# Optimization experiments

Measured on AMD Instinct MI355X. Metric: run time of the kernel, lower is better.

The kernel has to match this reference:

```python
import jax, jax.numpy as jnp
import numpy as np
import math

D_MODEL = 512
N_HEADS = 8
D_K = D_MODEL // N_HEADS
D_FF = 2048
EPS = 1e-6


def _layer_norm(x, gamma, beta):
    # Matches the torch module: unbiased std (ddof=1), divide by (std + eps)
    mean = jnp.mean(x, axis=-1, keepdims=True)
    std = jnp.std(x, axis=-1, ddof=1, keepdims=True)
    return gamma * (x - mean) / (std + EPS) + beta


def setup_inputs() -> dict:
    key = jax.random.key(0)
    ks = jax.random.split(key, 16)
    B, S = 4, 2048
    s_attn = 1.0 / math.sqrt(D_MODEL)
    s_ff1 = 1.0 / math.sqrt(D_MODEL)
    s_ff2 = 1.0 / math.sqrt(D_FF)
    inp = {
        "x": jax.random.normal(ks[0], (B, S, D_MODEL), dtype=jnp.float32),
        "mask": jnp.ones((1, 1, S, S), dtype=jnp.int32),
        "wq": jax.random.normal(ks[1], (D_MODEL, D_MODEL), jnp.float32) * s_attn,
        "bq": jnp.zeros((D_MODEL,), jnp.float32),
        "wk": jax.random.normal(ks[2], (D_MODEL, D_MODEL), jnp.float32) * s_attn,
        "bk": jnp.zeros((D_MODEL,), jnp.float32),
        "wv": jax.random.normal(ks[3], (D_MODEL, D_MODEL), jnp.float32) * s_attn,
        "bv": jnp.zeros((D_MODEL,), jnp.float32),
        "wo": jax.random.normal(ks[4], (D_MODEL, D_MODEL), jnp.float32) * s_attn,
        "bo": jnp.zeros((D_MODEL,), jnp.float32),
        "w1": jax.random.normal(ks[5], (D_MODEL, D_FF), jnp.float32) * s_ff1,
        "b1": jnp.zeros((D_FF,), jnp.float32),
        "w2": jax.random.normal(ks[6], (D_FF, D_MODEL), jnp.float32) * s_ff2,
        "b2": jnp.zeros((D_MODEL,), jnp.float32),
        "g1": jnp.ones((1, 1, D_MODEL), jnp.float32),
        "be1": jnp.zeros((1, 1, D_MODEL), jnp.float32),
        "g2": jnp.ones((1, 1, D_MODEL), jnp.float32),
        "be2": jnp.zeros((1, 1, D_MODEL), jnp.float32),
    }
    return inp


def reference(x, mask, wq, bq, wk, bk, wv, bv, wo, bo, w1, b1, w2, b2, g1, be1, g2, be2):
    B, S, _ = x.shape
    # --- residual 1: pre-norm self-attention ---
    xn = _layer_norm(x, g1, be1)
    q = (xn @ wq + bq).reshape(B, S, N_HEADS, D_K).transpose(0, 2, 1, 3)
    k = (xn @ wk + bk).reshape(B, S, N_HEADS, D_K).transpose(0, 2, 1, 3)
    v = (xn @ wv + bv).reshape(B, S, N_HEADS, D_K).transpose(0, 2, 1, 3)
    # NOTE: source uses floor division `//` by sqrt(d_k) (a faithful-ly kept bug)
    scores = jnp.floor_divide(jnp.einsum("bhqd,bhkd->bhqk", q, k), math.sqrt(D_K))
    scores = jnp.where(mask == 0, jnp.float32(-1e9), scores)
    attn = jax.nn.softmax(scores, axis=-1)
    ctx = jnp.einsum("bhqk,bhkd->bhqd", attn, v)
    ctx = ctx.transpose(0, 2, 1, 3).reshape(B, S, D_MODEL)
    x = x + (ctx @ wo + bo)
    # --- residual 2: pre-norm feed-forward ---
    xn2 = _layer_norm(x, g2, be2)
    ff = jax.nn.relu(xn2 @ w1 + b1) @ w2 + b2
    return x + ff
```

## Files before the change

### kernel.cpp

```cpp
#include <hip/hip_runtime.h>
#include <cmath>

#define SEQ 2048
#define DM 512
#define DFF 2048
#define NH 8
#define DKH 64
#define NROWS 8192

typedef __attribute__((ext_vector_type(8))) short bf16x8;
typedef __attribute__((ext_vector_type(16))) float f32x16;

__device__ __forceinline__ ushort f2bf(float f) {
    uint u = __float_as_uint(f);
    u += 0x7fff + ((u >> 16) & 1);
    return (ushort)(u >> 16);
}
__device__ __forceinline__ float bf2f(ushort h) {
    return __uint_as_float(((uint)h) << 16);
}
__device__ __forceinline__ uint cvtpk_bf16(float a, float b) {
    uint r;
    asm("v_cvt_pk_bf16_f32 %0, %1, %2" : "=v"(r) : "v"(a), "v"(b));
    return r;
}
__device__ __forceinline__ void gl_lds16(const void* g, void* l) {
    __builtin_amdgcn_global_load_lds(
        (const __attribute__((address_space(1))) void*)g,
        (__attribute__((address_space(3))) void*)l, 16, 0, 0);
}
__device__ __forceinline__ void* swz(char* base, int row, int col) {
    int byte = (row << 7) + (col << 1);
    byte ^= (row & 7) << 4;
    return base + byte;
}
__device__ __forceinline__ void* swzg(char* base, int row, int k) {
    int byte = (row << 7) + (k << 1);
    byte ^= ((row >> 2) & 7) << 4;
    return base + byte;
}

template<bool SPLIT>
__global__ __launch_bounds__(64) void ln_kernel(const float* __restrict__ x,
        const float* __restrict__ g, const float* __restrict__ b,
        ushort* __restrict__ oh, ushort* __restrict__ ol) {
    int row = blockIdx.x;
    int t = threadIdx.x;
    const float* xr = x + (size_t)row * DM + t * 8;
    float v[8];
    *(float4*)&v[0] = *(const float4*)(xr);
    *(float4*)&v[4] = *(const float4*)(xr + 4);
    float s = 0.f;
    #pragma unroll
    for (int j = 0; j < 8; ++j) s += v[j];
    #pragma unroll
    for (int m = 32; m > 0; m >>= 1) s += __shfl_xor(s, m);
    float mean = s * (1.0f / DM);
    float ss = 0.f;
    #pragma unroll
    for (int j = 0; j < 8; ++j) { float d = v[j] - mean; ss += d * d; }
    #pragma unroll
    for (int m = 32; m > 0; m >>= 1) ss += __shfl_xor(ss, m);
    float inv = 1.0f / (sqrtf(ss * (1.0f / (DM - 1))) + 1e-6f);
    float gv[8], bv[8];
    *(float4*)&gv[0] = *(const float4*)(g + t * 8);
    *(float4*)&gv[4] = *(const float4*)(g + t * 8 + 4);
    *(float4*)&bv[0] = *(const float4*)(b + t * 8);
    *(float4*)&bv[4] = *(const float4*)(b + t * 8 + 4);
    union { ushort us[8]; float4 f4; } ph, pl;
    #pragma unroll
    for (int j = 0; j < 8; ++j) {
        float o = gv[j] * (v[j] - mean) * inv + bv[j];
        ushort hb = f2bf(o);
        ph.us[j] = hb;
        if (SPLIT) pl.us[j] = f2bf(o - bf2f(hb));
    }
    *(float4*)(oh + (size_t)row * DM + t * 8) = ph.f4;
    if (SPLIT) *(float4*)(ol + (size_t)row * DM + t * 8) = pl.f4;
}

template<bool SPLIT>
__global__ __launch_bounds__(256) void wconv(const float* __restrict__ W,
        ushort* __restrict__ Th, ushort* __restrict__ Tl, int K, int N) {
    __shared__ float tile[64][65];
    int k0 = blockIdx.x * 64, n0 = blockIdx.y * 64;
    int t = threadIdx.x;
    {
        int kr = t >> 2, c0 = (t & 3) * 16;
        const float* src = W + (size_t)(k0 + kr) * N + n0 + c0;
        #pragma unroll
        for (int j = 0; j < 4; ++j)
            *(float4*)&tile[kr][c0 + j * 4] = *(const float4*)(src + j * 4);
    }
    __syncthreads();
    int n = t >> 2, kc = (t & 3) * 16;
    union { ushort us[16]; float4 f4[2]; } ph, pl;
    #pragma unroll
    for (int j = 0; j < 16; ++j) {
        float v = tile[kc + j][n];
        ushort hb = f2bf(v);
        ph.us[j] = hb;
        if (SPLIT) pl.us[j] = f2bf(v - bf2f(hb));
    }
    ushort* dh = Th + (size_t)(n0 + n) * K + k0 + kc;
    *(float4*)(dh) = ph.f4[0];
    *(float4*)(dh + 8) = ph.f4[1];
    if (SPLIT) {
        ushort* dl = Tl + (size_t)(n0 + n) * K + k0 + kc;
        *(float4*)(dl) = pl.f4[0];
        *(float4*)(dl + 8) = pl.f4[1];
    }
}

__global__ __launch_bounds__(256) void vtrans(const ushort* __restrict__ vh,
        ushort* __restrict__ vt) {
    __shared__ __align__(16) char tile[8192];
    int s0 = blockIdx.x * 64;
    int bh = blockIdx.y;
    int b = bh >> 3, h = bh & 7;
    int t = threadIdx.x;
    {
        int r = t >> 2, co = (t & 3) * 16;
        const ushort* src = vh + (size_t)(b * SEQ + s0 + r) * DM + h * DKH + co;
        *(float4*)swz(tile, r, co) = *(const float4*)(src);
        *(float4*)swz(tile, r, co + 8) = *(const float4*)(src + 8);
    }
    __syncthreads();
    int d = t >> 2, j0 = (t & 3) * 16;
    union { ushort us[16]; float4 f4[2]; } o;
    #pragma unroll
    for (int j = 0; j < 16; ++j)
        o.us[j] = *(ushort*)swz(tile, j0 + j, d);
    ushort* dst = vt + ((size_t)bh * DKH + d) * SEQ + s0 + j0;
    *(float4*)(dst) = o.f4[0];
    *(float4*)(dst + 8) = o.f4[1];
}

__global__ __launch_bounds__(256) void maskprep(const int* __restrict__ mask,
        ushort* __restrict__ mb) {
    int i = (blockIdx.x * 256 + threadIdx.x) * 8;
    int4 a = *(const int4*)(mask + i);
    int4 c = *(const int4*)(mask + i + 4);
    ushort neg = f2bf(-1e9f);
    union { ushort us[8]; float4 f4; } o;
    o.us[0] = a.x ? (ushort)0 : neg;
    o.us[1] = a.y ? (ushort)0 : neg;
    o.us[2] = a.z ? (ushort)0 : neg;
    o.us[3] = a.w ? (ushort)0 : neg;
    o.us[4] = c.x ? (ushort)0 : neg;
    o.us[5] = c.y ? (ushort)0 : neg;
    o.us[6] = c.z ? (ushort)0 : neg;
    o.us[7] = c.w ? (ushort)0 : neg;
    *(float4*)(mb + i) = o.f4;
}

template<bool RELU, bool HASRES, int OUT>
__global__ __launch_bounds__(256) void mgemm(
        const ushort* __restrict__ Ah, const ushort* __restrict__ Bth,
        const float* __restrict__ bias, const float* __restrict__ resid,
        float* __restrict__ Cf, ushort* __restrict__ Cbh,
        int M, int N, int K) {
    __shared__ __align__(16) char smem[65536];
    int tid = threadIdx.x;
    int lane = tid & 63, w = tid >> 6;
    int ln31 = lane & 31, hi = lane >> 5;
    int mh = (w >> 1) * 64, nh = (w & 1) * 64;
    int gx = gridDim.x;
    int nwg = gx * gridDim.y;
    int flat = blockIdx.y * gx + blockIdx.x;
    int sid = (flat & 7) * (nwg >> 3) + (flat >> 3);
    int n0 = (sid % gx) * 128;
    int m0 = (sid / gx) * 128;

    f32x16 acc[2][2];
    #pragma unroll
    for (int i = 0; i < 2; ++i)
        #pragma unroll
        for (int j = 0; j < 2; ++j)
            #pragma unroll
            for (int r = 0; r < 16; ++r) acc[i][j][r] = 0.f;

    auto stage = [&](char* Abuf, char* Bbuf, int k0) {
        #pragma unroll
        for (int c = 0; c < 4; ++c) {
            int ch = w * 4 + c;
            int r = ch * 8 + (lane >> 3);
            int u = (lane & 7) ^ ((r >> 2) & 7);
            gl_lds16(Ah + (size_t)(m0 + r) * K + k0 + u * 8, Abuf + ch * 1024);
            gl_lds16(Bth + (size_t)(n0 + r) * K + k0 + u * 8, Bbuf + ch * 1024);
        }
    };

    char* A0 = smem;
    char* B0 = smem + 16384;
    char* A1 = smem + 32768;
    char* B1 = smem + 49152;

    stage(A0, B0, 0);
    __syncthreads();
    int nk = K / 64;
    for (int kt = 0; kt < nk; ++kt) {
        char* Ac = (kt & 1) ? A1 : A0;
        char* Bc = (kt & 1) ? B1 : B0;
        if (kt + 1 < nk)
            stage((kt & 1) ? A0 : A1, (kt & 1) ? B0 : B1, (kt + 1) * 64);
        __builtin_amdgcn_s_setprio(1);
        #pragma unroll
        for (int km = 0; km < 4; ++km) {
            int kk = km * 16 + hi * 8;
            bf16x8 ah[2], bh[2];
            ah[0] = *(bf16x8*)swzg(Ac, mh + ln31, kk);
            ah[1] = *(bf16x8*)swzg(Ac, mh + 32 + ln31, kk);
            bh[0] = *(bf16x8*)swzg(Bc, nh + ln31, kk);
            bh[1] = *(bf16x8*)swzg(Bc, nh + 32 + ln31, kk);
            #pragma unroll
            for (int mi = 0; mi < 2; ++mi)
                #pragma unroll
                for (int ni = 0; ni < 2; ++ni)
                    acc[mi][ni] = __builtin_amdgcn_mfma_f32_32x32x16_bf16(
                        ah[mi], bh[ni], acc[mi][ni], 0, 0, 0);
        }
        __builtin_amdgcn_s_setprio(0);
        __syncthreads();
    }
    float bv[2];
    bv[0] = bias[n0 + nh + ln31];
    bv[1] = bias[n0 + nh + 32 + ln31];
    #pragma unroll
    for (int mi = 0; mi < 2; ++mi)
        #pragma unroll
        for (int ni = 0; ni < 2; ++ni) {
            int n = n0 + nh + ni * 32 + ln31;
            #pragma unroll
            for (int r = 0; r < 16; ++r) {
                int m = m0 + mh + mi * 32 + (r & 3) + 8 * (r >> 2) + 4 * hi;
                float v = acc[mi][ni][r] + bv[ni];
                if (HASRES) v += resid[(size_t)m * N + n];
                if (RELU) v = fmaxf(v, 0.f);
                size_t idx = (size_t)m * N + n;
                if (OUT == 0) Cf[idx] = v;
                else Cbh[idx] = f2bf(v);
            }
        }
}

__global__ __launch_bounds__(256) void qkv_gemm(
        const ushort* __restrict__ Ah, const ushort* __restrict__ Al,
        const ushort* __restrict__ Bth, const ushort* __restrict__ Btl,
        const float* __restrict__ bq, const float* __restrict__ bk,
        const float* __restrict__ bv_, ushort* __restrict__ q_h,
        ushort* __restrict__ q_l, ushort* __restrict__ k_h,
        ushort* __restrict__ k_l, ushort* __restrict__ v_h) {
    const int K = DM, N = DM;
    __shared__ __align__(16) char smem[65536];
    char* As_h = smem;
    char* Bs_h = smem + 16384;
    char* As_l = smem + 32768;
    char* Bs_l = smem + 49152;
    int tid = threadIdx.x;
    int lane = tid & 63, w = tid >> 6;
    int ln31 = lane & 31, hi = lane >> 5;
    int mh = (w >> 1) * 64, nh = (w & 1) * 64;
    int gx = gridDim.x;
    int nwg = gx * gridDim.y;
    int flat = blockIdx.y * gx + blockIdx.x;
    int sid = (flat & 7) * (nwg >> 3) + (flat >> 3);
    int n0 = (sid % gx) * 128;
    int m0 = (sid / gx) * 128;
    bool isqk = (n0 < 1024);

    f32x16 acc[2][2];
    #pragma unroll
    for (int i = 0; i < 2; ++i)
        #pragma unroll
        for (int j = 0; j < 2; ++j)
            #pragma unroll
            for (int r = 0; r < 16; ++r) acc[i][j][r] = 0.f;

    for (int k0 = 0; k0 < K; k0 += 64) {
        #pragma unroll
        for (int c = 0; c < 4; ++c) {
            int ch = w * 4 + c;
            int r = ch * 8 + (lane >> 3);
            int u = (lane & 7) ^ ((r >> 2) & 7);
            gl_lds16(Ah + (size_t)(m0 + r) * K + k0 + u * 8, As_h + ch * 1024);
            gl_lds16(Bth + (size_t)(n0 + r) * K + k0 + u * 8, Bs_h + ch * 1024);
            if (isqk) {
                gl_lds16(Al + (size_t)(m0 + r) * K + k0 + u * 8, As_l + ch * 1024);
                gl_lds16(Btl + (size_t)(n0 + r) * K + k0 + u * 8, Bs_l + ch * 1024);
            }
        }
        __syncthreads();
        __builtin_amdgcn_s_setprio(1);
        #pragma unroll
        for (int km = 0; km < 4; ++km) {
            int kk = km * 16 + hi * 8;
            bf16x8 ah[2], bh[2];
            ah[0] = *(bf16x8*)swzg(As_h, mh + ln31, kk);
            ah[1] = *(bf16x8*)swzg(As_h, mh + 32 + ln31, kk);
            bh[0] = *(bf16x8*)swzg(Bs_h, nh + ln31, kk);
            bh[1] = *(bf16x8*)swzg(Bs_h, nh + 32 + ln31, kk);
            if (isqk) {
                bf16x8 al[2], bl[2];
                al[0] = *(bf16x8*)swzg(As_l, mh + ln31, kk);
                al[1] = *(bf16x8*)swzg(As_l, mh + 32 + ln31, kk);
                bl[0] = *(bf16x8*)swzg(Bs_l, nh + ln31, kk);
                bl[1] = *(bf16x8*)swzg(Bs_l, nh + 32 + ln31, kk);
                #pragma unroll
                for (int mi = 0; mi < 2; ++mi)
                    #pragma unroll
                    for (int ni = 0; ni < 2; ++ni) {
                        acc[mi][ni] = __builtin_amdgcn_mfma_f32_32x32x16_bf16(
                            ah[mi], bh[ni], acc[mi][ni], 0, 0, 0);
                        acc[mi][ni] = __builtin_amdgcn_mfma_f32_32x32x16_bf16(
                            ah[mi], bl[ni], acc[mi][ni], 0, 0, 0);
                        acc[mi][ni] = __builtin_amdgcn_mfma_f32_32x32x16_bf16(
                            al[mi], bh[ni], acc[mi][ni], 0, 0, 0);
                    }
            } else {
                #pragma unroll
                for (int mi = 0; mi < 2; ++mi)
                    #pragma unroll
                    for (int ni = 0; ni < 2; ++ni)
                        acc[mi][ni] = __builtin_amdgcn_mfma_f32_32x32x16_bf16(
                            ah[mi], bh[ni], acc[mi][ni], 0, 0, 0);
            }
        }
        __builtin_amdgcn_s_setprio(0);
        __syncthreads();
    }
    const float* bias = (n0 < 512) ? bq : (n0 < 1024 ? bk : bv_);
    int ncol0 = n0 & 511;
    ushort* Oh = (n0 < 512) ? q_h : (n0 < 1024 ? k_h : v_h);
    ushort* Ol = (n0 < 512) ? q_l : (n0 < 1024 ? k_l : nullptr);
    float bvv[2];
    bvv[0] = bias[ncol0 + nh + ln31];
    bvv[1] = bias[ncol0 + nh + 32 + ln31];
    #pragma unroll
    for (int mi = 0; mi < 2; ++mi)
        #pragma unroll
        for (int ni = 0; ni < 2; ++ni) {
            int n = ncol0 + nh + ni * 32 + ln31;
            #pragma unroll
            for (int r = 0; r < 16; ++r) {
                int m = m0 + mh + mi * 32 + (r & 3) + 8 * (r >> 2) + 4 * hi;
                float v = acc[mi][ni][r] + bvv[ni];
                size_t idx = (size_t)m * N + n;
                ushort hb = f2bf(v);
                Oh[idx] = hb;
                if (isqk) Ol[idx] = f2bf(v - bf2f(hb));
            }
        }
}

__global__ __launch_bounds__(256, 2) void attn_kernel(
        const ushort* __restrict__ Qh, const ushort* __restrict__ Ql,
        const ushort* __restrict__ Khg, const ushort* __restrict__ Klg,
        const ushort* __restrict__ Vtg, const ushort* __restrict__ mb,
        ushort* __restrict__ O) {
    __shared__ __align__(16) char smem[65536];
    int tid = threadIdx.x;
    int w = tid >> 6, lane = tid & 63;
    int ln31 = lane & 31, hi = lane >> 5;
    int f = blockIdx.y * gridDim.x + blockIdx.x;
    int g = (f & 7) * 64 + (f >> 3);
    int qb = g & 15, bh = g >> 4;
    int b = bh >> 3, h = bh & 7;
    int q0 = qb * 128;
    size_t brow = (size_t)b * SEQ;
    int hcol = h * DKH;
    char* PqW = smem + 49152 + w * 4096;

    auto stage_kv = [&](char* buf, int kt) {
        #pragma unroll
        for (int c = 0; c < 2; ++c) {
            int ch = w * 2 + c;
            int r = ch * 8 + (lane >> 3);
            int u = (lane & 7) ^ (r & 7);
            gl_lds16(Khg + (brow + kt * 64 + r) * DM + hcol + u * 8,
                     buf + ch * 1024);
            gl_lds16(Klg + (brow + kt * 64 + r) * DM + hcol + u * 8,
                     buf + 8192 + ch * 1024);
            gl_lds16(Vtg + ((size_t)bh * DKH + r) * SEQ + kt * 64 + u * 8,
                     buf + 16384 + ch * 1024);
        }
    };

    stage_kv(smem, 0);
    {
        char* QhL = smem + 24576;
        char* QlL = smem + 40960;
        #pragma unroll
        for (int c = 0; c < 4; ++c) {
            int ch = w * 4 + c;
            int r = ch * 8 + (lane >> 3);
            int u = (lane & 7) ^ (r & 7);
            gl_lds16(Qh + (brow + q0 + r) * DM + hcol + u * 8, QhL + ch * 1024);
            gl_lds16(Ql + (brow + q0 + r) * DM + hcol + u * 8, QlL + ch * 1024);
        }
    }
    __syncthreads();
    bf16x8 qfh[4], qfl[4];
    {
        int qr = w * 32 + ln31;
        #pragma unroll
        for (int c = 0; c < 4; ++c) {
            qfh[c] = *(bf16x8*)swz(smem + 24576, qr, c * 16 + hi * 8);
            qfl[c] = *(bf16x8*)swz(smem + 40960, qr, c * 16 + hi * 8);
        }
    }
    __syncthreads();

    f32x16 ctx0, ctx1;
    #pragma unroll
    for (int r = 0; r < 16; ++r) { ctx0[r] = 0.f; ctx1[r] = 0.f; }
    float m_i = -1e30f, l_i = 0.f;
    int qglob = q0 + w * 32 + ln31;
    const ushort* mrow = mb + (size_t)qglob * SEQ;

    for (int kt = 0; kt < SEQ / 64; ++kt) {
        char* cur = smem + (kt & 1) * 24576;
        if (kt + 1 < SEQ / 64)
            stage_kv(smem + ((kt + 1) & 1) * 24576, kt + 1);
        char* KhL = cur;
        char* KlL = cur + 8192;
        char* VtL = cur + 16384;
        #pragma unroll
        for (int ksub = 0; ksub < 2; ++ksub) {
            f32x16 s;
            #pragma unroll
            for (int r = 0; r < 16; ++r) s[r] = 0.f;
            __builtin_amdgcn_s_setprio(1);
            #pragma unroll
            for (int c = 0; c < 4; ++c) {
                bf16x8 ka = *(bf16x8*)swz(KhL, ksub * 32 + ln31, c * 16 + hi * 8);
                bf16x8 kb = *(bf16x8*)swz(KlL, ksub * 32 + ln31, c * 16 + hi * 8);
                s = __builtin_amdgcn_mfma_f32_32x32x16_bf16(ka, qfh[c], s, 0, 0, 0);
                s = __builtin_amdgcn_mfma_f32_32x32x16_bf16(ka, qfl[c], s, 0, 0, 0);
                s = __builtin_amdgcn_mfma_f32_32x32x16_bf16(kb, qfh[c], s, 0, 0, 0);
            }
            __builtin_amdgcn_s_setprio(0);
            float tmax = -1e30f;
            #pragma unroll
            for (int rg = 0; rg < 4; ++rg) {
                ushort4 mv = *(const ushort4*)(mrow + kt * 64 + ksub * 32 + rg * 8 + hi * 4);
                ushort mu[4] = {mv.x, mv.y, mv.z, mv.w};
                #pragma unroll
                for (int j = 0; j < 4; ++j) {
                    int r = rg * 4 + j;
                    float sc = floorf(s[r] * 0.125f) + bf2f(mu[j]);
                    s[r] = sc;
                    tmax = fmaxf(tmax, sc);
                }
            }
            tmax = fmaxf(tmax, __shfl_xor(tmax, 32));
            if (!__all(tmax <= m_i)) {
                float newm = fmaxf(m_i, tmax);
                float scl = __expf(m_i - newm);
                m_i = newm;
                l_i *= scl;
                #pragma unroll
                for (int r = 0; r < 16; ++r) { ctx0[r] *= scl; ctx1[r] *= scl; }
            }
            float psum = 0.f;
            #pragma unroll
            for (int r = 0; r < 16; ++r) {
                float p = __expf(s[r] - m_i);
                s[r] = p;
                psum += p;
            }
            psum += __shfl_xor(psum, 32);
            l_i += psum;
            #pragma unroll
            for (int rg = 0; rg < 4; ++rg) {
                uint2 pk;
                pk.x = cvtpk_bf16(s[rg * 4 + 0], s[rg * 4 + 1]);
                pk.y = cvtpk_bf16(s[rg * 4 + 2], s[rg * 4 + 3]);
                *(uint2*)swz(PqW, ln31, ksub * 32 + rg * 8 + hi * 4) = pk;
            }
            __builtin_amdgcn_s_setprio(1);
            #pragma unroll
            for (int cc = 0; cc < 2; ++cc) {
                int c = ksub * 2 + cc;
                bf16x8 pb  = *(bf16x8*)swz(PqW, ln31, c * 16 + hi * 8);
                bf16x8 va0 = *(bf16x8*)swz(VtL, ln31, c * 16 + hi * 8);
                bf16x8 va1 = *(bf16x8*)swz(VtL, 32 + ln31, c * 16 + hi * 8);
                ctx0 = __builtin_amdgcn_mfma_f32_32x32x16_bf16(va0, pb, ctx0, 0, 0, 0);
                ctx1 = __builtin_amdgcn_mfma_f32_32x32x16_bf16(va1, pb, ctx1, 0, 0, 0);
            }
            __builtin_amdgcn_s_setprio(0);
        }
        __syncthreads();
    }

    float inv = 1.0f / l_i;
    ushort* op = O + (brow + qglob) * DM + hcol;
    #pragma unroll
    for (int r = 0; r < 16; ++r) {
        int d = (r & 3) + 8 * (r >> 2) + 4 * hi;
        op[d] = f2bf(ctx0[r] * inv);
        op[32 + d] = f2bf(ctx1[r] * inv);
    }
}

extern "C" void kernel_launch(void* const* d_in, const int* in_sizes, int n_in,
                              void* d_out, int out_size, void* d_ws, size_t ws_size,
                              hipStream_t stream) {
    const float* x    = (const float*)d_in[0];
    const int*   mask = (const int*)d_in[1];
    const float* wq = (const float*)d_in[2];
    const float* bq = (const float*)d_in[3];
    const float* wk = (const float*)d_in[4];
    const float* bk = (const float*)d_in[5];
    const float* wv = (const float*)d_in[6];
    const float* bv = (const float*)d_in[7];
    const float* wo = (const float*)d_in[8];
    const float* bo = (const float*)d_in[9];
    const float* w1 = (const float*)d_in[10];
    const float* b1 = (const float*)d_in[11];
    const float* w2 = (const float*)d_in[12];
    const float* b2 = (const float*)d_in[13];
    const float* g1  = (const float*)d_in[14];
    const float* be1 = (const float*)d_in[15];
    const float* g2  = (const float*)d_in[16];
    const float* be2 = (const float*)d_in[17];
    float* out = (float*)d_out;

    char* ws = (char*)d_ws;
    const size_t MiB = 1024 * 1024;
    ushort* xn_h = (ushort*)(ws);
    ushort* xn_l = (ushort*)(ws + 8 * MiB);
    ushort* q_h  = (ushort*)(ws + 16 * MiB);
    ushort* q_l  = (ushort*)(ws + 24 * MiB);
    ushort* k_h  = (ushort*)(ws + 32 * MiB);
    ushort* k_l  = (ushort*)(ws + 40 * MiB);
    ushort* v_h  = (ushort*)(ws + 48 * MiB);
    ushort* v_t  = (ushort*)(ws + 56 * MiB);
    ushort* wqkvt_h = (ushort*)(ws + 64 * MiB);
    ushort* wqkvt_l = (ushort*)(ws + 66 * MiB);
    ushort* wot_h = (ushort*)(ws + 67 * MiB);
    ushort* w1t_h = (ushort*)(ws + 68 * MiB);
    ushort* w2t_h = (ushort*)(ws + 70 * MiB);
    ushort* mb    = (ushort*)(ws + 72 * MiB);
    ushort* ctx  = xn_h;
    ushort* xn2  = xn_l;
    ushort* ff1  = q_h;

    dim3 blk256(256);
    wconv<true ><<<dim3(8, 8),  blk256, 0, stream>>>(wq, wqkvt_h, wqkvt_l, DM, DM);
    wconv<true ><<<dim3(8, 8),  blk256, 0, stream>>>(wk, wqkvt_h + 512 * 512, wqkvt_l + 512 * 512, DM, DM);
    wconv<false><<<dim3(8, 8),  blk256, 0, stream>>>(wv, wqkvt_h + 1024 * 512, nullptr, DM, DM);
    wconv<false><<<dim3(8, 8),  blk256, 0, stream>>>(wo, wot_h, nullptr, DM, DM);
    wconv<false><<<dim3(8, 32), blk256, 0, stream>>>(w1, w1t_h, nullptr, DM, DFF);
    wconv<false><<<dim3(32, 8), blk256, 0, stream>>>(w2, w2t_h, nullptr, DFF, DM);
    maskprep<<<SEQ * SEQ / 8 / 256, blk256, 0, stream>>>(mask, mb);
    ln_kernel<true><<<NROWS, 64, 0, stream>>>(x, g1, be1, xn_h, xn_l);
    qkv_gemm<<<dim3(12, NROWS / 128), blk256, 0, stream>>>(
        xn_h, xn_l, wqkvt_h, wqkvt_l, bq, bk, bv, q_h, q_l, k_h, k_l, v_h);
    vtrans<<<dim3(SEQ / 64, 4 * NH), blk256, 0, stream>>>(v_h, v_t);
    {
        dim3 grid(SEQ / 128, 4 * NH);
        attn_kernel<<<grid, blk256, 0, stream>>>(q_h, q_l, k_h, k_l, v_t, mb, ctx);
    }
    {
        dim3 grid(DM / 128, NROWS / 128);
        mgemm<false,true,0><<<grid, blk256, 0, stream>>>(
            ctx, wot_h, bo, x, out, nullptr, NROWS, DM, DM);
    }
    ln_kernel<false><<<NROWS, 64, 0, stream>>>(out, g2, be2, xn2, nullptr);
    {
        dim3 grid(DFF / 128, NROWS / 128);
        mgemm<true,false,1><<<grid, blk256, 0, stream>>>(
            xn2, w1t_h, b1, nullptr, nullptr, ff1, NROWS, DFF, DM);
    }
    {
        dim3 grid(DM / 128, NROWS / 128);
        mgemm<false,true,0><<<grid, blk256, 0, stream>>>(
            ff1, w2t_h, b2, out, out, nullptr, NROWS, DM, DFF);
    }
}
```

Measured before the change: 253.8 us.

## Shuffle P through registers in attention, cut LDS to 48KB, batch weight conversion

The attention kernel stops writing the probability tile P to shared memory. It now builds the MFMA B operand by exchanging packed bf16 halves between the two half-waves with a shuffle. This frees 16KB of LDS, so the kernel now uses 48KB and raises its launch bound to 3 blocks per CU; Q staging now reuses the K/V buffer region, with an extra barrier before the first K/V tile is staged. The mask values for each key tile are prefetched into registers before the QK MFMAs, and the four 512x512 weight conversions are merged into one 3D-grid launch. The trade-off is extra shuffle and select instructions and higher register pressure under the tighter launch bound.

```diff
diff --git a/kernel.cpp b/kernel.cpp
--- a/kernel.cpp
+++ b/kernel.cpp
@@ -79,10 +79,19 @@
     if (SPLIT) *(float4*)(ol + (size_t)row * DM + t * 8) = pl.f4;
 }
 
-template<bool SPLIT>
-__global__ __launch_bounds__(256) void wconv(const float* __restrict__ W,
-        ushort* __restrict__ Th, ushort* __restrict__ Tl, int K, int N) {
+__global__ __launch_bounds__(256) void wconv4(
+        const float* __restrict__ wq, const float* __restrict__ wk,
+        const float* __restrict__ wv, const float* __restrict__ wo,
+        ushort* __restrict__ qh, ushort* __restrict__ ql,
+        ushort* __restrict__ kh, ushort* __restrict__ kl,
+        ushort* __restrict__ vh, ushort* __restrict__ oh) {
+    const int K = DM, N = DM;
     __shared__ float tile[64][65];
+    int z = blockIdx.z;
+    const float* W = (z == 0) ? wq : (z == 1) ? wk : (z == 2) ? wv : wo;
+    ushort* Th = (z == 0) ? qh : (z == 1) ? kh : (z == 2) ? vh : oh;
+    ushort* Tl = (z == 0) ? ql : (z == 1) ? kl : nullptr;
+    bool split = (z < 2);
     int k0 = blockIdx.x * 64, n0 = blockIdx.y * 64;
     int t = threadIdx.x;
     {
@@ -100,16 +109,38 @@
         float v = tile[kc + j][n];
         ushort hb = f2bf(v);
         ph.us[j] = hb;
-        if (SPLIT) pl.us[j] = f2bf(v - bf2f(hb));
+        pl.us[j] = f2bf(v - bf2f(hb));
     }
     ushort* dh = Th + (size_t)(n0 + n) * K + k0 + kc;
     *(float4*)(dh) = ph.f4[0];
     *(float4*)(dh + 8) = ph.f4[1];
-    if (SPLIT) {
+    if (split) {
         ushort* dl = Tl + (size_t)(n0 + n) * K + k0 + kc;
         *(float4*)(dl) = pl.f4[0];
         *(float4*)(dl + 8) = pl.f4[1];
     }
+}
+
+__global__ __launch_bounds__(256) void wconv(const float* __restrict__ W,
+        ushort* __restrict__ Th, int K, int N) {
+    __shared__ float tile[64][65];
+    int k0 = blockIdx.x * 64, n0 = blockIdx.y * 64;
+    int t = threadIdx.x;
+    {
+        int kr = t >> 2, c0 = (t & 3) * 16;
+        const float* src = W + (size_t)(k0 + kr) * N + n0 + c0;
+        #pragma unroll
+        for (int j = 0; j < 4; ++j)
+            *(float4*)&tile[kr][c0 + j * 4] = *(const float4*)(src + j * 4);
+    }
+    __syncthreads();
+    int n = t >> 2, kc = (t & 3) * 16;
+    union { ushort us[16]; float4 f4[2]; } ph;
+    #pragma unroll
+    for (int j = 0; j < 16; ++j) ph.us[j] = f2bf(tile[kc + j][n]);
+    ushort* dh = Th + (size_t)(n0 + n) * K + k0 + kc;
+    *(float4*)(dh) = ph.f4[0];
+    *(float4*)(dh + 8) = ph.f4[1];
 }
 
 __global__ __launch_bounds__(256) void vtrans(const ushort* __restrict__ vh,
@@ -353,15 +384,16 @@
         }
 }
 
-__global__ __launch_bounds__(256, 2) void attn_kernel(
+__global__ __launch_bounds__(256, 3) void attn_kernel(
         const ushort* __restrict__ Qh, const ushort* __restrict__ Ql,
         const ushort* __restrict__ Khg, const ushort* __restrict__ Klg,
         const ushort* __restrict__ Vtg, const ushort* __restrict__ mb,
         ushort* __restrict__ O) {
-    __shared__ __align__(16) char smem[65536];
+    __shared__ __align__(16) char smem[49152];
     int tid = threadIdx.x;
     int w = tid >> 6, lane = tid & 63;
     int ln31 = lane & 31, hi = lane >> 5;
+    bool hib = (hi != 0);
     int f = blockIdx.y * gridDim.x + blockIdx.x;
     int g = (f & 7) * 64 + (f >> 3);
     int qb = g & 15, bh = g >> 4;
@@ -369,7 +401,6 @@
     int q0 = qb * 128;
     size_t brow = (size_t)b * SEQ;
     int hcol = h * DKH;
-    char* PqW = smem + 49152 + w * 4096;
 
     auto stage_kv = [&](char* buf, int kt) {
         #pragma unroll
@@ -386,10 +417,9 @@
         }
     };
 
-    stage_kv(smem, 0);
-    {
-        char* QhL = smem + 24576;
-        char* QlL = smem + 40960;
+    {
+        char* QhL = smem;
+        char* QlL = smem + 16384;
         #pragma unroll
         for (int c = 0; c < 4; ++c) {
             int ch = w * 4 + c;
@@ -405,10 +435,12 @@
         int qr = w * 32 + ln31;
         #pragma unroll
         for (int c = 0; c < 4; ++c) {
-            qfh[c] = *(bf16x8*)swz(smem + 24576, qr, c * 16 + hi * 8);
-            qfl[c] = *(bf16x8*)swz(smem + 40960, qr, c * 16 + hi * 8);
-        }
-    }
+            qfh[c] = *(bf16x8*)swz(smem, qr, c * 16 + hi * 8);
+            qfl[c] = *(bf16x8*)swz(smem + 16384, qr, c * 16 + hi * 8);
+        }
+    }
+    __syncthreads();
+    stage_kv(smem, 0);
     __syncthreads();
 
     f32x16 ctx0, ctx1;
@@ -422,6 +454,10 @@
         char* cur = smem + (kt & 1) * 24576;
         if (kt + 1 < SEQ / 64)
             stage_kv(smem + ((kt + 1) & 1) * 24576, kt + 1);
+        ushort4 mpre[8];
+        #pragma unroll
+        for (int i = 0; i < 8; ++i)
+            mpre[i] = *(const ushort4*)(mrow + kt * 64 + i * 8 + hi * 4);
         char* KhL = cur;
         char* KlL = cur + 8192;
         char* VtL = cur + 16384;
@@ -443,7 +479,7 @@
             float tmax = -1e30f;
             #pragma unroll
             for (int rg = 0; rg < 4; ++rg) {
-                ushort4 mv = *(const ushort4*)(mrow + kt * 64 + ksub * 32 + rg * 8 + hi * 4);
+                ushort4 mv = mpre[ksub * 4 + rg];
                 ushort mu[4] = {mv.x, mv.y, mv.z, mv.w};
                 #pragma unroll
                 for (int j = 0; j < 4; ++j) {
@@ -471,22 +507,33 @@
             }
             psum += __shfl_xor(psum, 32);
             l_i += psum;
+            uint pk0[4], pk1[4];
             #pragma unroll
             for (int rg = 0; rg < 4; ++rg) {
-                uint2 pk;
-                pk.x = cvtpk_bf16(s[rg * 4 + 0], s[rg * 4 + 1]);
-                pk.y = cvtpk_bf16(s[rg * 4 + 2], s[rg * 4 + 3]);
-                *(uint2*)swz(PqW, ln31, ksub * 32 + rg * 8 + hi * 4) = pk;
+                pk0[rg] = cvtpk_bf16(s[rg * 4 + 0], s[rg * 4 + 1]);
+                pk1[rg] = cvtpk_bf16(s[rg * 4 + 2], s[rg * 4 + 3]);
             }
             __builtin_amdgcn_s_setprio(1);
             #pragma unroll
             for (int cc = 0; cc < 2; ++cc) {
+                uint A0 = pk0[cc * 2], A1 = pk1[cc * 2];
+                uint B0 = pk0[cc * 2 + 1], B1 = pk1[cc * 2 + 1];
+                uint send0 = hib ? A0 : B0;
+                uint send1 = hib ? A1 : B1;
+                uint own0  = hib ? B0 : A0;
+                uint own1  = hib ? B1 : A1;
+                uint recv0 = (uint)__shfl_xor((int)send0, 32);
+                uint recv1 = (uint)__shfl_xor((int)send1, 32);
+                union { uint u[4]; bf16x8 v; } pb;
+                pb.u[0] = hib ? recv0 : own0;
+                pb.u[1] = hib ? recv1 : own1;
+                pb.u[2] = hib ? own0 : recv0;
+                pb.u[3] = hib ? own1 : recv1;
                 int c = ksub * 2 + cc;
-                bf16x8 pb  = *(bf16x8*)swz(PqW, ln31, c * 16 + hi * 8);
                 bf16x8 va0 = *(bf16x8*)swz(VtL, ln31, c * 16 + hi * 8);
                 bf16x8 va1 = *(bf16x8*)swz(VtL, 32 + ln31, c * 16 + hi * 8);
-                ctx0 = __builtin_amdgcn_mfma_f32_32x32x16_bf16(va0, pb, ctx0, 0, 0, 0);
-                ctx1 = __builtin_amdgcn_mfma_f32_32x32x16_bf16(va1, pb, ctx1, 0, 0, 0);
+                ctx0 = __builtin_amdgcn_mfma_f32_32x32x16_bf16(va0, pb.v, ctx0, 0, 0, 0);
+                ctx1 = __builtin_amdgcn_mfma_f32_32x32x16_bf16(va1, pb.v, ctx1, 0, 0, 0);
             }
             __builtin_amdgcn_s_setprio(0);
         }
@@ -547,12 +594,11 @@
     ushort* ff1  = q_h;
 
     dim3 blk256(256);
-    wconv<true ><<<dim3(8, 8),  blk256, 0, stream>>>(wq, wqkvt_h, wqkvt_l, DM, DM);
-    wconv<true ><<<dim3(8, 8),  blk256, 0, stream>>>(wk, wqkvt_h + 512 * 512, wqkvt_l + 512 * 512, DM, DM);
-    wconv<false><<<dim3(8, 8),  blk256, 0, stream>>>(wv, wqkvt_h + 1024 * 512, nullptr, DM, DM);
-    wconv<false><<<dim3(8, 8),  blk256, 0, stream>>>(wo, wot_h, nullptr, DM, DM);
-    wconv<false><<<dim3(8, 32), blk256, 0, stream>>>(w1, w1t_h, nullptr, DM, DFF);
-    wconv<false><<<dim3(32, 8), blk256, 0, stream>>>(w2, w2t_h, nullptr, DFF, DM);
+    wconv4<<<dim3(8, 8, 4), blk256, 0, stream>>>(
+        wq, wk, wv, wo, wqkvt_h, wqkvt_l, wqkvt_h + 512 * 512,
+        wqkvt_l + 512 * 512, wqkvt_h + 1024 * 512, wot_h);
+    wconv<<<dim3(8, 32), blk256, 0, stream>>>(w1, w1t_h, DM, DFF);
+    wconv<<<dim3(32, 8), blk256, 0, stream>>>(w2, w2t_h, DFF, DM);
     maskprep<<<SEQ * SEQ / 8 / 256, blk256, 0, stream>>>(mask, mb);
     ln_kernel<true><<<NROWS, 64, 0, stream>>>(x, g1, be1, xn_h, xn_l);
     qkv_gemm<<<dim3(12, NROWS / 128), blk256, 0, stream>>>(
```

Measured after the change: 240.7 us. 5.1% less time.
